# Kernel optimization log

Hardware: AMD Instinct MI355X
Metric: run time of the kernel (lower is better)

## Reference

```python
import jax, jax.numpy as jnp
import numpy as np

H, D, K, FF = 4, 256, 1024, 1024  # n_head, d_model, key_feature_dim, dim_feedforward
L, B = 2048, 4                    # pixels, batch


def setup_inputs() -> dict:
    key = jax.random.key(0)
    ks = jax.random.split(key, 12)
    def g(k, shape, s=0.02):
        return jax.random.normal(k, shape, jnp.float32) * s
    return dict(
        src=jax.random.normal(ks[0], (L, B, D), jnp.float32),
        WK=g(ks[1], (H, K, D), (2.0 / K) ** 0.5),
        WQ=g(ks[2], (H, K, D), (2.0 / K) ** 0.5),
        WV=g(ks[3], (H, D, D), (2.0 / D) ** 0.5),
        TC=g(ks[4], (H, D, D)),
        ENw1=g(ks[5], (H, FF, D)), ENb1=jnp.zeros((H, FF), jnp.float32),
        ENw2=g(ks[6], (H, D, FF)), ENb2=jnp.zeros((H, D), jnp.float32),
        ENg=jnp.ones((H, D), jnp.float32), ENbeta=jnp.zeros((H, D), jnp.float32),
        Wout=g(ks[7], (D, H * D)),
        L1w=g(ks[8], (FF, D)), L1b=jnp.zeros((FF,), jnp.float32),
        L2w=g(ks[9], (D, FF)), L2b=jnp.zeros((D,), jnp.float32),
        N1g=jnp.ones((D,), jnp.float32), N1b=jnp.zeros((D,), jnp.float32),
        N2g=jnp.ones((D,), jnp.float32), N2b=jnp.zeros((D,), jnp.float32),
    )


def _ln(x, g, b, eps=1e-5):
    m = jnp.mean(x, -1, keepdims=True)
    v = jnp.mean((x - m) ** 2, -1, keepdims=True)
    return (x - m) * jax.lax.rsqrt(v + eps) * g + b


def _l2n(x, eps=1e-12):
    n = jnp.sqrt(jnp.sum(x * x, -1, keepdims=True))
    return x / jnp.maximum(n, eps)


def reference(src, WK, WQ, WV, TC, ENw1, ENb1, ENw2, ENb2, ENg, ENbeta,
              Wout, L1w, L1b, L2w, L2b, N1g, N1b, N2g, N2b):
    # --- RMA: per-head RelationUnit, vectorized over head axis h ---
    wq = _l2n(jnp.einsum('lbd,hkd->hlbk', src, WQ))   # (H,L,B,K), L2-normed
    wk = _l2n(jnp.einsum('lbd,hkd->hlbk', src, WK))
    wv = jnp.einsum('lbd,hed->hlbe', src, WV)         # (H,L,B,D)
    dot = jnp.einsum('hlbk,hmbk->hblm', wq, wk)       # (H,B,Lq,Lk)
    aff = jax.nn.softmax(dot, axis=-1)                 # softmax over keys (temp=1)
    aff = aff / (1e-9 + jnp.sum(aff, axis=2, keepdims=True))  # renorm over QUERY dim (torch dim=1)
    out = jnp.einsum('hblm,hmbe->hlbe', aff, wv)       # (H,L,B,D)
    ru = jax.nn.relu(jnp.einsum('hlbe,hfe->hlbf', src[None] - out, TC))
    # per-head extra TransNonlinear: residual MLP + layernorm
    hid = jax.nn.relu(jnp.einsum('hlbd,hfd->hlbf', ru, ENw1) + ENb1[:, None, None, :])
    s2 = jnp.einsum('hlbf,hdf->hlbd', hid, ENw2) + ENb2[:, None, None, :]
    tn = _ln(ru + s2, ENg[:, None, None, :], ENbeta[:, None, None, :])  # (H,L,B,D)
    concat = jnp.transpose(tn, (1, 2, 0, 3)).reshape(L, B, H * D)
    attn = concat @ Wout.T                              # (L,B,D)
    # --- encoder layer: residual + LN + FFN + LN (dropout = eval identity) ---
    x = _ln(src + attn, N1g, N1b)
    ff = jax.nn.relu(x @ L1w.T + L1b) @ L2w.T + L2b
    return _ln(x + ff, N2g, N2b)
```

## Files before the change

kernel.cpp:

```cpp
#include <hip/hip_runtime.h>
#include <hip/hip_bf16.h>

typedef __hip_bfloat16 bf16;
typedef short s16x8 __attribute__((ext_vector_type(8)));
typedef float f32x4 __attribute__((ext_vector_type(4)));

#define HN 4
#define DM 256
#define KF 1024
#define FFD 1024
#define LL 2048
#define BB 4
#define NN (LL * BB)
#define HD (HN * DM)

__device__ __forceinline__ float b2f(unsigned short u) {
    unsigned v = ((unsigned)u) << 16; float f; __builtin_memcpy(&f, &v, 4); return f;
}
__device__ __forceinline__ unsigned short f2b(float f) {
    bf16 b = (bf16)f; unsigned short u; __builtin_memcpy(&u, &b, 2); return u;
}

__device__ __forceinline__ float waveReduceSum(float v) {
    for (int o = 32; o; o >>= 1) v += __shfl_down(v, o, 64);
    return v;
}
__device__ __forceinline__ float waveReduceMax(float v) {
    for (int o = 32; o; o >>= 1) v = fmaxf(v, __shfl_down(v, o, 64));
    return v;
}
__device__ __forceinline__ float blockReduceSum(float v) {
    __shared__ float sh[4];
    v = waveReduceSum(v);
    __syncthreads();
    if ((threadIdx.x & 63) == 0) sh[threadIdx.x >> 6] = v;
    __syncthreads();
    return sh[0] + sh[1] + sh[2] + sh[3];
}
__device__ __forceinline__ float blockReduceMax(float v) {
    __shared__ float sh[4];
    v = waveReduceMax(v);
    __syncthreads();
    if ((threadIdx.x & 63) == 0) sh[threadIdx.x >> 6] = v;
    __syncthreads();
    return fmaxf(fmaxf(sh[0], sh[1]), fmaxf(sh[2], sh[3]));
}

__global__ void sentinel_kernel(float* out, float val) {
    if (threadIdx.x == 0 && blockIdx.x == 0) out[0] = val;
}

__device__ __forceinline__ void gll16(const void* g, void* l) {
#if defined(__HIP_DEVICE_COMPILE__)
    __builtin_amdgcn_global_load_lds(
        (const __attribute__((address_space(1))) unsigned int*)g,
        (__attribute__((address_space(3))) unsigned int*)l, 16, 0, 0);
#endif
}

#define VMC(n) asm volatile("s_waitcnt vmcnt(" #n ")" ::: "memory")
#define LGKM0() asm volatile("s_waitcnt lgkmcnt(0)" ::: "memory")

__device__ __forceinline__ void xcd_swz(int& bx, int& by) {
    int gx = gridDim.x;
    int n2 = gx * gridDim.y;
    if ((n2 & 7) == 0) {
        int f = bx + by * gx;
        int fs = (f & 7) * (n2 >> 3) + (f >> 3);
        bx = fs % gx;
        by = fs / gx;
    }
}

__global__ __launch_bounds__(512) void gemm256(
    const bf16* __restrict__ A, int lda, long sA,
    const bf16* __restrict__ Bv, int ldb, long sB,
    void* __restrict__ C, int cF32, int ldc, long sC,
    int Kc,
    const float* __restrict__ bias, long sBias,
    const void* __restrict__ aux, int auxType, int ldaux, long sAux,
    float accSign, int relu, int swz)
{
    const int z = blockIdx.z;
    const bf16* Ah = A + (long)z * sA;
    const bf16* Bh = Bv + (long)z * sB;
    float* Cf = (float*)C + (long)z * sC;
    bf16*  Ch = (bf16*)C + (long)z * sC;
    const float* biasp = bias ? (bias + (long)z * sBias) : nullptr;
    const float* auxf = (auxType == 1) ? ((const float*)aux + (long)z * sAux) : nullptr;
    const bf16*  auxh = (auxType == 2) ? ((const bf16*)aux + (long)z * sAux) : nullptr;

    __shared__ __align__(16) bf16 As[2][256 * 64];
    __shared__ __align__(16) bf16 Bs[2][256 * 64];

    const int tid  = threadIdx.x;
    const int lane = tid & 63;
    const int wid  = __builtin_amdgcn_readfirstlane(tid >> 6);
    const int wm   = wid >> 2;
    const int wn   = wid & 3;
    const int lrow = lane & 15;
    const int quad = lane >> 4;
    int bx = blockIdx.x, by = blockIdx.y;
    if (swz) xcd_swz(bx, by);
    const int m0 = bx * 256;
    const int n0 = by * 256;

    const int srow8  = wid * 8 + (lane >> 3);
    const int scolsw = ((lane & 7) * 8) ^ ((srow8 & 7) << 3);
    const bf16* Aorg = Ah + (long)m0 * lda;
    const bf16* Borg = Bh + (long)n0 * ldb;

    const int colx = (lane & 7) << 3;
    const int kc0 = (quad * 8) ^ colx;
    const int kc1 = (32 + quad * 8) ^ colx;

    f32x4 acc[8][4] = {};
    s16x8 afr[4][2], bfr[4][2];

    const int nk = Kc >> 6;

    auto stg = [&](const bf16* org, int ld, bf16* lds, int k0, int h) {
#pragma unroll
        for (int j = 0; j < 2; j++) {
            int rl = h * 128 + j * 64 + srow8;
            gll16((const void*)(org + (long)rl * ld + k0 + scolsw),
                  (void*)(lds + (h * 128 + j * 64 + wid * 8) * 64));
        }
    };

    stg(Aorg, lda, As[0], 0, 0); stg(Aorg, lda, As[0], 0, 1);
    stg(Borg, ldb, Bs[0], 0, 0); stg(Borg, ldb, Bs[0], 0, 1);
    if (nk > 1) {
        stg(Aorg, lda, As[1], 64, 0); stg(Aorg, lda, As[1], 64, 1);
        stg(Borg, ldb, Bs[1], 64, 0); stg(Borg, ldb, Bs[1], 64, 1);
        VMC(8);
    } else {
        VMC(0);
    }
    __builtin_amdgcn_s_barrier();

    for (int t = 0; t < nk; ++t) {
        const int s = t & 1;
        const bf16* Acur = As[s];
        const bf16* Bcur = Bs[s];
        bf16* Anxt = As[s ^ 1];
        bf16* Bslot = Bs[s];
        const bool stA = (t >= 1) && (t + 1 < nk);
        const bool stB = (t + 2 < nk);

#pragma unroll
        for (int mi = 0; mi < 4; mi++) {
            int r = (wm * 128 + mi * 16 + lrow) * 64;
            afr[mi][0] = *(const s16x8*)&Acur[r + kc0];
            afr[mi][1] = *(const s16x8*)&Acur[r + kc1];
        }
#pragma unroll
        for (int ni = 0; ni < 2; ni++) {
            int r = (wn * 64 + ni * 16 + lrow) * 64;
            bfr[ni][0] = *(const s16x8*)&Bcur[r + kc0];
            bfr[ni][1] = *(const s16x8*)&Bcur[r + kc1];
        }
        if (stA) stg(Aorg, lda, Anxt, (t + 1) << 6, 0);
        __builtin_amdgcn_s_barrier();
        LGKM0();
        __builtin_amdgcn_s_setprio(1);
#pragma unroll
        for (int mi = 0; mi < 4; mi++)
#pragma unroll
            for (int ni = 0; ni < 2; ni++)
#pragma unroll
                for (int ks = 0; ks < 2; ks++)
                    acc[mi][ni] = __builtin_amdgcn_mfma_f32_16x16x32_bf16(afr[mi][ks], bfr[ni][ks], acc[mi][ni], 0, 0, 0);
        __builtin_amdgcn_s_setprio(0);
        __builtin_amdgcn_s_barrier();

#pragma unroll
        for (int ni = 0; ni < 2; ni++) {
            int r = (wn * 64 + (2 + ni) * 16 + lrow) * 64;
            bfr[2 + ni][0] = *(const s16x8*)&Bcur[r + kc0];
            bfr[2 + ni][1] = *(const s16x8*)&Bcur[r + kc1];
        }
        if (stA) stg(Aorg, lda, Anxt, (t + 1) << 6, 1);
        __builtin_amdgcn_s_barrier();
        LGKM0();
        __builtin_amdgcn_s_setprio(1);
#pragma unroll
        for (int mi = 0; mi < 4; mi++)
#pragma unroll
            for (int ni = 0; ni < 2; ni++)
#pragma unroll
                for (int ks = 0; ks < 2; ks++)
                    acc[mi][2 + ni] = __builtin_amdgcn_mfma_f32_16x16x32_bf16(afr[mi][ks], bfr[2 + ni][ks], acc[mi][2 + ni], 0, 0, 0);
        __builtin_amdgcn_s_setprio(0);
        __builtin_amdgcn_s_barrier();

#pragma unroll
        for (int mi = 0; mi < 4; mi++) {
            int r = (wm * 128 + 64 + mi * 16 + lrow) * 64;
            afr[mi][0] = *(const s16x8*)&Acur[r + kc0];
            afr[mi][1] = *(const s16x8*)&Acur[r + kc1];
        }
        if (stB) stg(Borg, ldb, Bslot, (t + 2) << 6, 0);
        __builtin_amdgcn_s_barrier();
        LGKM0();
        __builtin_amdgcn_s_setprio(1);
#pragma unroll
        for (int mi = 0; mi < 4; mi++)
#pragma unroll
            for (int ni = 0; ni < 2; ni++)
#pragma unroll
                for (int ks = 0; ks < 2; ks++)
                    acc[4 + mi][ni] = __builtin_amdgcn_mfma_f32_16x16x32_bf16(afr[mi][ks], bfr[ni][ks], acc[4 + mi][ni], 0, 0, 0);
        __builtin_amdgcn_s_setprio(0);
        __builtin_amdgcn_s_barrier();

        if (stB) stg(Borg, ldb, Bslot, (t + 2) << 6, 1);
        __builtin_amdgcn_s_barrier();
        __builtin_amdgcn_s_setprio(1);
#pragma unroll
        for (int mi = 0; mi < 4; mi++)
#pragma unroll
            for (int ni = 0; ni < 2; ni++)
#pragma unroll
                for (int ks = 0; ks < 2; ks++)
                    acc[4 + mi][2 + ni] = __builtin_amdgcn_mfma_f32_16x16x32_bf16(afr[mi][ks], bfr[2 + ni][ks], acc[4 + mi][2 + ni], 0, 0, 0);
        __builtin_amdgcn_s_setprio(0);
        if (stB) { VMC(4); } else { VMC(0); }
        __builtin_amdgcn_s_barrier();
    }

#pragma unroll
    for (int mi = 0; mi < 8; mi++) {
#pragma unroll
        for (int ni = 0; ni < 4; ni++) {
            int col = n0 + wn * 64 + ni * 16 + lrow;
            float bvl = biasp ? biasp[col] : 0.0f;
#pragma unroll
            for (int i = 0; i < 4; i++) {
                int row = m0 + wm * 128 + mi * 16 + quad * 4 + i;
                float v = accSign * acc[mi][ni][i] + bvl;
                if (auxType == 1) v += auxf[(long)row * ldaux + col];
                else if (auxType == 2) v += (float)auxh[(long)row * ldaux + col];
                if (relu) v = fmaxf(v, 0.0f);
                if (cF32) Cf[(long)row * ldc + col] = v;
                else Ch[(long)row * ldc + col] = (bf16)v;
            }
        }
    }
}

template<int BN>
__global__ __launch_bounds__(256) void gemm_nt(
    const void* __restrict__ A, int aF32, int lda, long sA,
    const void* __restrict__ Bv, int bF32, int ldb, long sB,
    void* __restrict__ C, int cF32, int ldc, long sC,
    int Kc,
    const float* __restrict__ bias, long sBias,
    const void* __restrict__ aux, int auxType, int ldaux, long sAux,
    float accSign, int relu)
{
    constexpr int NI = BN / 32;
    constexpr int WN = BN / 2;
    const int z = blockIdx.z;
    const float* Af = (const float*)A + (long)z * sA;
    const bf16*  Ah = (const bf16*)A + (long)z * sA;
    const float* Bf = (const float*)Bv + (long)z * sB;
    const bf16*  Bh = (const bf16*)Bv + (long)z * sB;
    float* Cf = (float*)C + (long)z * sC;
    bf16*  Ch = (bf16*)C + (long)z * sC;
    const float* biasp = bias ? (bias + (long)z * sBias) : nullptr;
    const float* auxf = (auxType == 1) ? ((const float*)aux + (long)z * sAux) : nullptr;
    const bf16*  auxh = (auxType == 2) ? ((const bf16*)aux + (long)z * sAux) : nullptr;

    __shared__ __align__(16) bf16 As[3][128 * 32];
    __shared__ __align__(16) bf16 Bs[3][BN * 32];

    const int tid = threadIdx.x;
    const int lane = tid & 63;
    const int wv = __builtin_amdgcn_readfirstlane(tid >> 6);
    const int wm = (tid >> 6) & 1;
    const int wn = (tid >> 6) >> 1;
    const int lrow = lane & 15;
    const int quad = lane >> 4;
    const int m0 = blockIdx.x * 128;
    const int n0 = blockIdx.y * BN;
    const int srow = tid >> 1;
    const int scol = (tid & 1) * 16;
    const int drow = wv * 16 + (lane >> 2);
    const int dcol = (lane & 3) * 8;

    f32x4 acc[4][NI] = {};

    if (!aF32 && !bF32) {
        const int nk = Kc >> 5;
        auto stage = [&](int t) {
            const int buf = t % 3;
            const int k0 = t << 5;
            const bf16* a0 = Ah + (long)(m0 + drow) * lda + k0 + dcol;
            gll16((const void*)a0, (void*)&As[buf][wv * 512]);
            gll16((const void*)(a0 + (long)lda * 64), (void*)&As[buf][2048 + wv * 512]);
            const bf16* b0 = Bh + (long)(n0 + drow) * ldb + k0 + dcol;
            gll16((const void*)b0, (void*)&Bs[buf][wv * 512]);
            if (BN == 128)
                gll16((const void*)(b0 + (long)ldb * 64), (void*)&Bs[buf][2048 + wv * 512]);
        };
        stage(0);
        if (nk > 1) {
            stage(1);
            if constexpr (BN == 128) { VMC(4); } else { VMC(3); }
        } else {
            VMC(0);
        }
        __builtin_amdgcn_s_barrier();
        for (int t = 0; t < nk; ++t) {
            const int cur = t % 3;
            if (t + 2 < nk) stage(t + 2);
            s16x8 af[4], bfg[NI];
#pragma unroll
            for (int mi = 0; mi < 4; mi++)
                af[mi] = *(const s16x8*)&As[cur][(wm * 64 + mi * 16 + lrow) * 32 + quad * 8];
#pragma unroll
            for (int ni = 0; ni < NI; ni++)
                bfg[ni] = *(const s16x8*)&Bs[cur][(wn * WN + ni * 16 + lrow) * 32 + quad * 8];
#pragma unroll
            for (int mi = 0; mi < 4; mi++)
#pragma unroll
                for (int ni = 0; ni < NI; ni++)
                    acc[mi][ni] = __builtin_amdgcn_mfma_f32_16x16x32_bf16(af[mi], bfg[ni], acc[mi][ni], 0, 0, 0);
            if (t + 2 < nk) {
                if constexpr (BN == 128) { VMC(4); } else { VMC(3); }
            } else {
                VMC(0);
            }
            __builtin_amdgcn_s_barrier();
        }
    } else {
        for (int k0 = 0; k0 < Kc; k0 += 32) {
            uint4 av0, av1, bv0, bv1;
            if (aF32) {
                const float* ag = Af + (long)(m0 + srow) * lda + k0 + scol;
                ushort t[16];
#pragma unroll
                for (int j = 0; j < 4; j++) {
                    float4 f = *(const float4*)(ag + 4 * j);
                    t[4*j] = f2b(f.x); t[4*j+1] = f2b(f.y); t[4*j+2] = f2b(f.z); t[4*j+3] = f2b(f.w);
                }
                av0 = *(const uint4*)&t[0]; av1 = *(const uint4*)&t[8];
            }
            if (bF32) {
                if (srow < BN) {
                    const float* bg = Bf + (long)(n0 + srow) * ldb + k0 + scol;
                    ushort t[16];
#pragma unroll
                    for (int j = 0; j < 4; j++) {
                        float4 f = *(const float4*)(bg + 4 * j);
                        t[4*j] = f2b(f.x); t[4*j+1] = f2b(f.y); t[4*j+2] = f2b(f.z); t[4*j+3] = f2b(f.w);
                    }
                    bv0 = *(const uint4*)&t[0]; bv1 = *(const uint4*)&t[8];
                }
            }
            __syncthreads();
            if (aF32) {
                *(uint4*)&As[0][srow * 32 + scol] = av0;
                *(uint4*)&As[0][srow * 32 + scol + 8] = av1;
            } else {
                gll16((const void*)(Ah + (long)(m0 + drow) * lda + k0 + dcol), (void*)&As[0][wv * 512]);
                gll16((const void*)(Ah + (long)(m0 + 64 + drow) * lda + k0 + dcol), (void*)&As[0][2048 + wv * 512]);
            }
            if (bF32) {
                if (srow < BN) {
                    *(uint4*)&Bs[0][srow * 32 + scol] = bv0;
                    *(uint4*)&Bs[0][srow * 32 + scol + 8] = bv1;
                }
            } else {
                gll16((const void*)(Bh + (long)(n0 + drow) * ldb + k0 + dcol), (void*)&Bs[0][wv * 512]);
                if (BN == 128)
                    gll16((const void*)(Bh + (long)(n0 + 64 + drow) * ldb + k0 + dcol), (void*)&Bs[0][2048 + wv * 512]);
            }
            __syncthreads();

            s16x8 af[4], bfg[NI];
#pragma unroll
            for (int mi = 0; mi < 4; mi++)
                af[mi] = *(const s16x8*)&As[0][(wm * 64 + mi * 16 + lrow) * 32 + quad * 8];
#pragma unroll
            for (int ni = 0; ni < NI; ni++)
                bfg[ni] = *(const s16x8*)&Bs[0][(wn * WN + ni * 16 + lrow) * 32 + quad * 8];
#pragma unroll
            for (int mi = 0; mi < 4; mi++)
#pragma unroll
                for (int ni = 0; ni < NI; ni++)
                    acc[mi][ni] = __builtin_amdgcn_mfma_f32_16x16x32_bf16(af[mi], bfg[ni], acc[mi][ni], 0, 0, 0);
        }
    }

#pragma unroll
    for (int mi = 0; mi < 4; mi++) {
#pragma unroll
        for (int ni = 0; ni < NI; ni++) {
            int col = n0 + wn * WN + ni * 16 + lrow;
            float bvl = biasp ? biasp[col] : 0.0f;
#pragma unroll
            for (int i = 0; i < 4; i++) {
                int row = m0 + wm * 64 + mi * 16 + quad * 4 + i;
                float v = accSign * acc[mi][ni][i] + bvl;
                if (auxType == 1) v += auxf[(long)row * ldaux + col];
                else if (auxType == 2) v += (float)auxh[(long)row * ldaux + col];
                if (relu) v = fmaxf(v, 0.0f);
                if (cF32) Cf[(long)row * ldc + col] = v;
                else Ch[(long)row * ldc + col] = (bf16)v;
            }
        }
    }
}

__global__ __launch_bounds__(256) void cvt4(const float* __restrict__ in, bf16* __restrict__ out, int n4) {
    int i = blockIdx.x * 256 + threadIdx.x;
    if (i < n4) {
        float4 f = ((const float4*)in)[i];
        ushort4 u; u.x = f2b(f.x); u.y = f2b(f.y); u.z = f2b(f.z); u.w = f2b(f.w);
        ((ushort4*)out)[i] = u;
    }
}

struct WCvt {
    const float* in[16];
    bf16* out[16];
    int n4[16];
};
__global__ __launch_bounds__(256) void cvt_weights(WCvt wc) {
    int t = blockIdx.y;
    int n4 = wc.n4[t];
    const float4* in = (const float4*)wc.in[t];
    ushort4* out = (ushort4*)wc.out[t];
    for (int i = blockIdx.x * 256 + threadIdx.x; i < n4; i += gridDim.x * 256) {
        float4 f = in[i];
        ushort4 u; u.x = f2b(f.x); u.y = f2b(f.y); u.z = f2b(f.z); u.w = f2b(f.w);
        out[i] = u;
    }
}

__global__ __launch_bounds__(256) void l2norm_rows(bf16* __restrict__ Q) {
    bf16* q = Q + (long)blockIdx.x * KF;
    ushort4 u = ((ushort4*)q)[threadIdx.x];
    float v0 = b2f(u.x), v1 = b2f(u.y), v2 = b2f(u.z), v3 = b2f(u.w);
    float ss = blockReduceSum(v0 * v0 + v1 * v1 + v2 * v2 + v3 * v3);
    float inv = 1.0f / fmaxf(sqrtf(ss), 1e-12f);
    u.x = f2b(v0 * inv); u.y = f2b(v1 * inv); u.z = f2b(v2 * inv); u.w = f2b(v3 * inv);
    ((ushort4*)q)[threadIdx.x] = u;
}

__global__ __launch_bounds__(256) void l2norm2(bf16* __restrict__ QK) {
    bf16* q = QK + (long)blockIdx.y * ((long)NN * KF) + (long)blockIdx.x * KF;
    ushort4 u = ((ushort4*)q)[threadIdx.x];
    float v0 = b2f(u.x), v1 = b2f(u.y), v2 = b2f(u.z), v3 = b2f(u.w);
    float ss = blockReduceSum(v0 * v0 + v1 * v1 + v2 * v2 + v3 * v3);
    float inv = 1.0f / fmaxf(sqrtf(ss), 1e-12f);
    u.x = f2b(v0 * inv); u.y = f2b(v1 * inv); u.z = f2b(v2 * inv); u.w = f2b(v3 * inv);
    ((ushort4*)q)[threadIdx.x] = u;
}

__global__ __launch_bounds__(256) void softmax_rows(bf16* __restrict__ P) {
    bf16* p = P + (long)blockIdx.x * LL;
    ushort4 a = ((ushort4*)p)[2 * threadIdx.x];
    ushort4 b = ((ushort4*)p)[2 * threadIdx.x + 1];
    float v[8] = {b2f(a.x), b2f(a.y), b2f(a.z), b2f(a.w), b2f(b.x), b2f(b.y), b2f(b.z), b2f(b.w)};
    float mx = -1e30f;
#pragma unroll
    for (int i = 0; i < 8; i++) mx = fmaxf(mx, v[i]);
    mx = blockReduceMax(mx);
    float s = 0.0f;
#pragma unroll
    for (int i = 0; i < 8; i++) { v[i] = __expf(v[i] - mx); s += v[i]; }
    s = blockReduceSum(s);
    float inv = 1.0f / s;
    a.x = f2b(v[0]*inv); a.y = f2b(v[1]*inv); a.z = f2b(v[2]*inv); a.w = f2b(v[3]*inv);
    b.x = f2b(v[4]*inv); b.y = f2b(v[5]*inv); b.z = f2b(v[6]*inv); b.w = f2b(v[7]*inv);
    ((ushort4*)p)[2 * threadIdx.x] = a;
    ((ushort4*)p)[2 * threadIdx.x + 1] = b;
}

__global__ __launch_bounds__(256) void zero_cs(float* __restrict__ cs) {
    cs[blockIdx.x * 256 + threadIdx.x] = 0.0f;
}

__global__ __launch_bounds__(256) void colsum2(const bf16* __restrict__ P, float* __restrict__ cs) {
    int col = blockIdx.x * 256 + threadIdx.x;
    int rc = blockIdx.y;
    int b = blockIdx.z;
    const bf16* p = P + (long)b * LL * LL + (long)rc * 128 * LL + col;
    float s = 0.0f;
#pragma unroll 4
    for (int r = 0; r < 128; r++) s += (float)p[(long)r * LL];
    atomicAdd(&cs[(long)b * LL + col], s);
}

__global__ __launch_bounds__(256) void scale_vt(bf16* __restrict__ vt, const float* __restrict__ cs) {
    int e = blockIdx.x, b = blockIdx.y;
    bf16* row = vt + ((long)b * DM + e) * LL;
    const float* c = cs + (long)b * LL;
#pragma unroll
    for (int i = 0; i < 8; i++) {
        int m = threadIdx.x + i * 256;
        row[m] = (bf16)((float)row[m] / (1e-9f + c[m]));
    }
}

__global__ __launch_bounds__(256) void ln_rows(const bf16* __restrict__ in, void* __restrict__ out,
                                               int outF32,
                                               const float* __restrict__ g, const float* __restrict__ b,
                                               const float* __restrict__ aux) {
    long base = (long)blockIdx.x * 256;
    float v = (float)in[base + threadIdx.x];
    if (aux) v += aux[base + threadIdx.x];
    float mean = blockReduceSum(v) * (1.0f / 256.0f);
    float d = v - mean;
    float var = blockReduceSum(d * d) * (1.0f / 256.0f);
    float o = d * rsqrtf(var + 1e-5f) * g[threadIdx.x] + b[threadIdx.x];
    if (outF32) ((float*)out)[base + threadIdx.x] = o;
    else ((bf16*)out)[base + threadIdx.x] = (bf16)o;
}

__global__ __launch_bounds__(256) void ln_cat(bf16* __restrict__ cat, const float* __restrict__ g,
                                              const float* __restrict__ bb) {
    long n = blockIdx.x;
    int h = blockIdx.y;
    bf16* x = cat + n * HD + (long)h * DM;
    float v = (float)x[threadIdx.x];
    float mean = blockReduceSum(v) * (1.0f / 256.0f);
    float d = v - mean;
    float var = blockReduceSum(d * d) * (1.0f / 256.0f);
    x[threadIdx.x] = (bf16)(d * rsqrtf(var + 1e-5f) * g[h * DM + threadIdx.x] + bb[h * DM + threadIdx.x]);
}

extern "C" void kernel_launch(void* const* d_in, const int* in_sizes, int n_in,
                              void* d_out, int out_size, void* d_ws, size_t ws_size,
                              hipStream_t stream) {
    const float* src  = (const float*)d_in[0];
    const float* WK   = (const float*)d_in[1];
    const float* WQ   = (const float*)d_in[2];
    const float* WV   = (const float*)d_in[3];
    const float* TC   = (const float*)d_in[4];
    const float* ENw1 = (const float*)d_in[5];
    const float* ENb1 = (const float*)d_in[6];
    const float* ENw2 = (const float*)d_in[7];
    const float* ENb2 = (const float*)d_in[8];
    const float* ENg  = (const float*)d_in[9];
    const float* ENbt = (const float*)d_in[10];
    const float* Wout = (const float*)d_in[11];
    const float* L1w  = (const float*)d_in[12];
    const float* L1b  = (const float*)d_in[13];
    const float* L2w  = (const float*)d_in[14];
    const float* L2b  = (const float*)d_in[15];
    const float* N1g  = (const float*)d_in[16];
    const float* N1b  = (const float*)d_in[17];
    const float* N2g  = (const float*)d_in[18];
    const float* N2b  = (const float*)d_in[19];

    const size_t COMPACT_FLOOR = 34700000;
    const size_t FAST_FLOOR  = 92307456;
    const size_t FASTW_FLOOR = 92307456 + 11010048;
    if (ws_size < COMPACT_FLOOR || out_size != NN * DM || n_in != 20) {
        float val;
        if (n_in != 20) val = 32768.0f + (float)n_in;
        else if (out_size != NN * DM) val = 49152.0f;
        else val = 16384.0f + 128.0f * (float)(unsigned)(ws_size >> 20);
        sentinel_kernel<<<1, 64, 0, stream>>>((float*)d_out, val);
        return;
    }

    char* w = (char*)d_ws;
    auto G = [&](const void* A, int aF, int lda, long sA,
                 const void* B, int bF, int ldb, long sB,
                 void* C, int cF, int ldc, long sC,
                 int M, int Nn, int Kc, int nb,
                 const float* bias, long sBias,
                 const void* aux, int auxT, int ldaux, long sAux,
                 float sgn, int relu) {
        gemm_nt<128><<<dim3(M / 128, Nn / 128, nb), dim3(256), 0, stream>>>(
            A, aF, lda, sA, B, bF, ldb, sB, C, cF, ldc, sC, Kc,
            bias, sBias, aux, auxT, ldaux, sAux, sgn, relu);
    };
    auto G64 = [&](const void* A, int aF, int lda, long sA,
                 const void* B, int bF, int ldb, long sB,
                 void* C, int cF, int ldc, long sC,
                 int M, int Nn, int Kc, int nb,
                 const float* bias, long sBias,
                 const void* aux, int auxT, int ldaux, long sAux,
                 float sgn, int relu) {
        gemm_nt<64><<<dim3(M / 128, Nn / 64, nb), dim3(256), 0, stream>>>(
            A, aF, lda, sA, B, bF, ldb, sB, C, cF, ldc, sC, Kc,
            bias, sBias, aux, auxT, ldaux, sAux, sgn, relu);
    };
    auto G2 = [&](const void* A, int lda, long sA,
                  const void* B, int ldb, long sB,
                  void* C, int cF, int ldc, long sC,
                  int M, int Nn, int Kc, int nb,
                  const float* bias, long sBias,
                  const void* aux, int auxT, int ldaux, long sAux,
                  float sgn, int relu) {
        gemm256<<<dim3(M / 256, Nn / 256, nb), dim3(512), 0, stream>>>(
            (const bf16*)A, lda, sA, (const bf16*)B, ldb, sB, C, cF, ldc, sC, Kc,
            bias, sBias, aux, auxT, ldaux, sAux, sgn, relu, 1);
    };

    if (ws_size >= FAST_FLOOR) {
        bf16*  Sb  = (bf16*)(w + 0);
        bf16*  Q   = (bf16*)(w + 4194304);
        bf16*  K   = (bf16*)(w + 20971520);
        bf16*  Vt  = (bf16*)(w + 37748736);
        bf16*  P   = (bf16*)(w + 41943040);
        bf16*  Su  = (bf16*)(w + 75497472);
        float* Cs  = (float*)(w + 92274688);
        bf16* Ru = Q; bf16* Hid = K; bf16* Cat = P;
        bf16* Attn = Vt; bf16* Xln = Su; bf16* Ffh = Q; bf16* Yp = Vt;

        const int haveWb = (ws_size >= FASTW_FLOOR) ? 1 : 0;
        char* wb = w + 92307456;
        bf16* WQKb  = (bf16*)(wb + 0);
        bf16* WVb   = (bf16*)(wb + 4194304);
        bf16* TCb   = (bf16*)(wb + 4718592);
        bf16* ENw1b = (bf16*)(wb + 5242880);
        bf16* ENw2b = (bf16*)(wb + 7340032);
        bf16* Woutb = (bf16*)(wb + 9437184);
        bf16* L1wb  = (bf16*)(wb + 9961472);
        bf16* L2wb  = (bf16*)(wb + 10485760);
        if (haveWb) {
            WCvt wc;
            for (int h = 0; h < HN; h++) {
                wc.in[2*h]   = WQ + (long)h * KF * DM; wc.out[2*h]   = WQKb + (long)h * 2048 * DM;            wc.n4[2*h]   = 65536;
                wc.in[2*h+1] = WK + (long)h * KF * DM; wc.out[2*h+1] = WQKb + (long)h * 2048 * DM + KF * DM;  wc.n4[2*h+1] = 65536;
            }
            wc.in[8]  = WV;   wc.out[8]  = WVb;   wc.n4[8]  = 65536;
            wc.in[9]  = TC;   wc.out[9]  = TCb;   wc.n4[9]  = 65536;
            wc.in[10] = ENw1; wc.out[10] = ENw1b; wc.n4[10] = 262144;
            wc.in[11] = ENw2; wc.out[11] = ENw2b; wc.n4[11] = 262144;
            wc.in[12] = Wout; wc.out[12] = Woutb; wc.n4[12] = 65536;
            wc.in[13] = L1w;  wc.out[13] = L1wb;  wc.n4[13] = 65536;
            wc.in[14] = L2w;  wc.out[14] = L2wb;  wc.n4[14] = 65536;
            cvt_weights<<<dim3(256, 15), 256, 0, stream>>>(wc);
        }
        const int wF = haveWb ? 0 : 1;
        auto WP = [&](const void* f32p, const void* b16p, long off) {
            return haveWb ? (const void*)((const bf16*)b16p + off)
                          : (const void*)((const float*)f32p + off);
        };

        cvt4<<<2048, 256, 0, stream>>>(src, Sb, NN * DM / 4);

        for (int h = 0; h < HN; h++) {
            if (haveWb) {
                G2(Sb, DM, 0, WQKb + (long)h * 2048 * DM, DM, (long)KF * DM,
                   Q, 0, KF, (long)NN * KF,
                   NN, KF, DM, 2, nullptr, 0, nullptr, 0, 0, 0, 1.0f, 0);
            } else {
                G(Sb, 0, DM, 0, WQ + (long)h * KF * DM, 1, DM, 0, Q, 0, KF, 0,
                  NN, KF, DM, 1, nullptr, 0, nullptr, 0, 0, 0, 1.0f, 0);
                G(Sb, 0, DM, 0, WK + (long)h * KF * DM, 1, DM, 0, K, 0, KF, 0,
                  NN, KF, DM, 1, nullptr, 0, nullptr, 0, 0, 0, 1.0f, 0);
            }
            G64(WP(WV, WVb, (long)h * DM * DM), wF, DM, 0, Sb, 0, BB * DM, DM,
              Vt, 0, LL, (long)DM * LL,
              DM, LL, DM, BB, nullptr, 0, nullptr, 0, 0, 0, 1.0f, 0);
            l2norm2<<<dim3(NN, 2), 256, 0, stream>>>(Q);
            G2(Q, BB * KF, KF, K, BB * KF, KF, P, 0, LL, (long)LL * LL,
               LL, LL, KF, BB, nullptr, 0, nullptr, 0, 0, 0, 1.0f, 0);
            softmax_rows<<<BB * LL, 256, 0, stream>>>(P);
            zero_cs<<<BB * LL / 256, 256, 0, stream>>>(Cs);
            colsum2<<<dim3(LL / 256, 16, BB), 256, 0, stream>>>(P, Cs);
            scale_vt<<<dim3(DM, BB), 256, 0, stream>>>(Vt, Cs);
            G64(P, 0, LL, (long)LL * LL, Vt, 0, LL, (long)DM * LL,
              Su + (long)h * NN * DM, 0, BB * DM, DM,
              LL, DM, LL, BB, nullptr, 0, Sb, 2, BB * DM, DM, -1.0f, 0);
        }
        G(Su, 0, DM, (long)NN * DM, WP(TC, TCb, 0), wF, DM, (long)DM * DM,
          Ru, 0, DM, (long)NN * DM,
          NN, DM, DM, HN, nullptr, 0, nullptr, 0, 0, 0, 1.0f, 1);
        for (int h = 0; h < HN; h++) {
            G(Ru + (long)h * NN * DM, 0, DM, 0, WP(ENw1, ENw1b, (long)h * FFD * DM), wF, DM, 0,
              Hid, 0, FFD, 0, NN, FFD, DM, 1, ENb1 + (long)h * FFD, 0, nullptr, 0, 0, 0, 1.0f, 1);
            G64(Hid, 0, FFD, 0, WP(ENw2, ENw2b, (long)h * DM * FFD), wF, FFD, 0,
              Cat + (long)h * DM, 0, HD, 0, NN, DM, FFD, 1,
              ENb2 + (long)h * DM, 0, Ru + (long)h * NN * DM, 2, DM, 0, 1.0f, 0);
        }
        ln_cat<<<dim3(NN, HN), 256, 0, stream>>>(Cat, ENg, ENbt);
        G64(Cat, 0, HD, 0, WP(Wout, Woutb, 0), wF, HD, 0, Attn, 0, DM, 0,
          NN, DM, HD, 1, nullptr, 0, nullptr, 0, 0, 0, 1.0f, 0);
        ln_rows<<<NN, 256, 0, stream>>>(Attn, Xln, 0, N1g, N1b, src);
        G(Xln, 0, DM, 0, WP(L1w, L1wb, 0), wF, DM, 0, Ffh, 0, FFD, 0,
          NN, FFD, DM, 1, L1b, 0, nullptr, 0, 0, 0, 1.0f, 1);
        G64(Ffh, 0, FFD, 0, WP(L2w, L2wb, 0), wF, FFD, 0, Yp, 0, DM, 0,
          NN, DM, FFD, 1, L2b, 0, Xln, 2, DM, 0, 1.0f, 0);
        ln_rows<<<NN, 256, 0, stream>>>(Yp, (float*)d_out, 1, N2g, N2b, nullptr);
    } else {
        bf16*  S0 = (bf16*)(w + 0);
        bf16*  S1 = (bf16*)(w + 16777216);
        bf16*  S2 = (bf16*)(w + 20971520);
        bf16*  S3 = (bf16*)(w + 25165824);
        bf16*  S4 = (bf16*)(w + 26214400);
        bf16*  S5 = (bf16*)(w + 30408704);
        float* Cs = (float*)(w + 34603008);

        for (int h = 0; h < HN; h++) {
            for (int b = 0; b < BB; b++) {
                G(src + b * DM, 1, BB * DM, 0, WQ + (long)h * KF * DM, 1, DM, 0,
                  S1, 0, KF, 0, LL, KF, DM, 1, nullptr, 0, nullptr, 0, 0, 0, 1.0f, 0);
                G(src + b * DM, 1, BB * DM, 0, WK + (long)h * KF * DM, 1, DM, 0,
                  S2, 0, KF, 0, LL, KF, DM, 1, nullptr, 0, nullptr, 0, 0, 0, 1.0f, 0);
                G(WV + (long)h * DM * DM, 1, DM, 0, src + b * DM, 1, BB * DM, 0,
                  S3, 0, LL, 0, DM, LL, DM, 1, nullptr, 0, nullptr, 0, 0, 0, 1.0f, 0);
                l2norm_rows<<<LL, 256, 0, stream>>>(S1);
                l2norm_rows<<<LL, 256, 0, stream>>>(S2);
                G(S1, 0, KF, 0, S2, 0, KF, 0, S0, 0, LL, 0,
                  LL, LL, KF, 1, nullptr, 0, nullptr, 0, 0, 0, 1.0f, 0);
                softmax_rows<<<LL, 256, 0, stream>>>(S0);
                zero_cs<<<LL / 256, 256, 0, stream>>>(Cs);
                colsum2<<<dim3(LL / 256, 16, 1), 256, 0, stream>>>(S0, Cs);
                scale_vt<<<dim3(DM, 1), 256, 0, stream>>>(S3, Cs);
                G(S0, 0, LL, 0, S3, 0, LL, 0, S4 + b * DM, 0, BB * DM, 0,
                  LL, DM, LL, 1, nullptr, 0, src + b * DM, 1, BB * DM, 0, -1.0f, 0);
            }
            G(S4, 0, DM, 0, TC + (long)h * DM * DM, 1, DM, 0, S1, 0, DM, 0,
              NN, DM, DM, 1, nullptr, 0, nullptr, 0, 0, 0, 1.0f, 1);
            G(S1, 0, DM, 0, ENw1 + (long)h * FFD * DM, 1, DM, 0, S0, 0, FFD, 0,
              NN, FFD, DM, 1, ENb1 + (long)h * FFD, 0, nullptr, 0, 0, 0, 1.0f, 1);
            G(S0, 0, FFD, 0, ENw2 + (long)h * DM * FFD, 1, FFD, 0, S2, 0, DM, 0,
              NN, DM, FFD, 1, ENb2 + (long)h * DM, 0, S1, 2, DM, 0, 1.0f, 0);
            ln_rows<<<NN, 256, 0, stream>>>(S2, S2, 0, ENg + (long)h * DM, ENbt + (long)h * DM, nullptr);
            G(S2, 0, DM, 0, Wout + (long)h * DM, 1, HD, 0, S5, 0, DM, 0,
              NN, DM, DM, 1, nullptr, 0, (h == 0) ? nullptr : (const void*)S5,
              (h == 0) ? 0 : 2, DM, 0, 1.0f, 0);
        }
        ln_rows<<<NN, 256, 0, stream>>>(S5, S1, 0, N1g, N1b, src);
        G(S1, 0, DM, 0, L1w, 1, DM, 0, S0, 0, FFD, 0,
          NN, FFD, DM, 1, L1b, 0, nullptr, 0, 0, 0, 1.0f, 1);
        G(S0, 0, FFD, 0, L2w, 1, FFD, 0, S2, 0, DM, 0,
          NN, DM, FFD, 1, L2b, 0, S1, 2, DM, 0, 1.0f, 0);
        ln_rows<<<NN, 256, 0, stream>>>(S2, (float*)d_out, 1, N2g, N2b, nullptr);
    }
}
```

Measured before the change: 1.042 ms.

## Defer L2 normalization into QK^T GEMM epilogue and add custom block swizzle

Instead of rewriting Q and K in place after L2 normalization, a rownorm kernel now only computes inverse row norms into a scratch float buffer (the output buffer). The QK^T GEMM epilogue scales each dot product by the query and key inverse norms. This removes the normalized bf16 write-back pass over Q/K. A dedicated tile remap for the 8x8 grid is also added to improve L2/XCD locality. The unnormalized bf16 inputs to the GEMM change rounding slightly, and reusing d_out as scratch relies on it being overwritten later.

```diff
diff --git a/kernel.cpp b/kernel.cpp
--- a/kernel.cpp
+++ b/kernel.cpp
@@ -79,7 +79,8 @@
     int Kc,
     const float* __restrict__ bias, long sBias,
     const void* __restrict__ aux, int auxType, int ldaux, long sAux,
-    float accSign, int relu, int swz)
+    float accSign, int relu,
+    const float* __restrict__ rqs, const float* __restrict__ rks, int swz)
 {
     const int z = blockIdx.z;
     const bf16* Ah = A + (long)z * sA;
@@ -101,7 +102,14 @@
     const int lrow = lane & 15;
     const int quad = lane >> 4;
     int bx = blockIdx.x, by = blockIdx.y;
-    if (swz) xcd_swz(bx, by);
+    if (swz == 2 && gridDim.x == 8 && gridDim.y == 8) {
+        int f = bx + (by << 3);
+        int c = f & 7, j = f >> 3;
+        by = ((c >> 1) << 1) | (j >> 2);
+        bx = ((c & 1) << 2) | (j & 3);
+    } else if (swz) {
+        xcd_swz(bx, by);
+    }
     const int m0 = bx * 256;
     const int n0 = by * 256;
 
@@ -235,10 +243,13 @@
         for (int ni = 0; ni < 4; ni++) {
             int col = n0 + wn * 64 + ni * 16 + lrow;
             float bvl = biasp ? biasp[col] : 0.0f;
+            float ck = rks ? rks[((long)col << 2) + z] : 1.0f;
 #pragma unroll
             for (int i = 0; i < 4; i++) {
                 int row = m0 + wm * 128 + mi * 16 + quad * 4 + i;
-                float v = accSign * acc[mi][ni][i] + bvl;
+                float v = accSign * acc[mi][ni][i];
+                if (rqs) v *= rqs[((long)row << 2) + z] * ck;
+                v += bvl;
                 if (auxType == 1) v += auxf[(long)row * ldaux + col];
                 else if (auxType == 2) v += (float)auxh[(long)row * ldaux + col];
                 if (relu) v = fmaxf(v, 0.0f);
@@ -450,14 +461,13 @@
     ((ushort4*)q)[threadIdx.x] = u;
 }
 
-__global__ __launch_bounds__(256) void l2norm2(bf16* __restrict__ QK) {
-    bf16* q = QK + (long)blockIdx.y * ((long)NN * KF) + (long)blockIdx.x * KF;
+__global__ __launch_bounds__(256) void rownorm(const bf16* __restrict__ QK, float* __restrict__ R) {
+    const bf16* q = QK + (long)blockIdx.y * ((long)NN * KF) + (long)blockIdx.x * KF;
     ushort4 u = ((ushort4*)q)[threadIdx.x];
     float v0 = b2f(u.x), v1 = b2f(u.y), v2 = b2f(u.z), v3 = b2f(u.w);
     float ss = blockReduceSum(v0 * v0 + v1 * v1 + v2 * v2 + v3 * v3);
-    float inv = 1.0f / fmaxf(sqrtf(ss), 1e-12f);
-    u.x = f2b(v0 * inv); u.y = f2b(v1 * inv); u.z = f2b(v2 * inv); u.w = f2b(v3 * inv);
-    ((ushort4*)q)[threadIdx.x] = u;
+    if (threadIdx.x == 0)
+        R[(long)blockIdx.y * NN + blockIdx.x] = 1.0f / fmaxf(sqrtf(ss), 1e-12f);
 }
 
 __global__ __launch_bounds__(256) void softmax_rows(bf16* __restrict__ P) {
@@ -598,10 +608,11 @@
                   int M, int Nn, int Kc, int nb,
                   const float* bias, long sBias,
                   const void* aux, int auxT, int ldaux, long sAux,
-                  float sgn, int relu) {
+                  float sgn, int relu,
+                  const float* rqs, const float* rks, int swz) {
         gemm256<<<dim3(M / 256, Nn / 256, nb), dim3(512), 0, stream>>>(
             (const bf16*)A, lda, sA, (const bf16*)B, ldb, sB, C, cF, ldc, sC, Kc,
-            bias, sBias, aux, auxT, ldaux, sAux, sgn, relu, 1);
+            bias, sBias, aux, auxT, ldaux, sAux, sgn, relu, rqs, rks, swz);
     };
 
     if (ws_size >= FAST_FLOOR) {
@@ -614,6 +625,8 @@
         float* Cs  = (float*)(w + 92274688);
         bf16* Ru = Q; bf16* Hid = K; bf16* Cat = P;
         bf16* Attn = Vt; bf16* Xln = Su; bf16* Ffh = Q; bf16* Yp = Vt;
+        float* RQ = (float*)d_out;
+        float* RK = RQ + NN;
 
         const int haveWb = (ws_size >= FASTW_FLOOR) ? 1 : 0;
         char* wb = w + 92307456;
@@ -652,7 +665,8 @@
             if (haveWb) {
                 G2(Sb, DM, 0, WQKb + (long)h * 2048 * DM, DM, (long)KF * DM,
                    Q, 0, KF, (long)NN * KF,
-                   NN, KF, DM, 2, nullptr, 0, nullptr, 0, 0, 0, 1.0f, 0);
+                   NN, KF, DM, 2, nullptr, 0, nullptr, 0, 0, 0, 1.0f, 0,
+                   nullptr, nullptr, 1);
             } else {
                 G(Sb, 0, DM, 0, WQ + (long)h * KF * DM, 1, DM, 0, Q, 0, KF, 0,
                   NN, KF, DM, 1, nullptr, 0, nullptr, 0, 0, 0, 1.0f, 0);
@@ -662,9 +676,10 @@
             G64(WP(WV, WVb, (long)h * DM * DM), wF, DM, 0, Sb, 0, BB * DM, DM,
               Vt, 0, LL, (long)DM * LL,
               DM, LL, DM, BB, nullptr, 0, nullptr, 0, 0, 0, 1.0f, 0);
-            l2norm2<<<dim3(NN, 2), 256, 0, stream>>>(Q);
+            rownorm<<<dim3(NN, 2), 256, 0, stream>>>(Q, RQ);
             G2(Q, BB * KF, KF, K, BB * KF, KF, P, 0, LL, (long)LL * LL,
-               LL, LL, KF, BB, nullptr, 0, nullptr, 0, 0, 0, 1.0f, 0);
+               LL, LL, KF, BB, nullptr, 0, nullptr, 0, 0, 0, 1.0f, 0,
+               RQ, RK, 2);
             softmax_rows<<<BB * LL, 256, 0, stream>>>(P);
             zero_cs<<<BB * LL / 256, 256, 0, stream>>>(Cs);
             colsum2<<<dim3(LL / 256, 16, BB), 256, 0, stream>>>(P, Cs);
```

New measurement: 1.113 ms. 1.07x slower.
